# Kernel optimization log

Hardware: AMD Instinct MI355X
Metric: run time of the kernel (lower is better)

## Reference

```python
import jax, jax.numpy as jnp
import numpy as np

N = 50000
E = 800000
C = 128          # in = hidden = out channels
R = 16           # num_relations
NB = 4           # num_bases
EPS = 1e-5


def setup_inputs() -> dict:
    key = jax.random.key(0)
    ks = jax.random.split(key, 20)
    node_features = jax.random.normal(ks[0], (N, C), dtype=jnp.float32)
    src = jax.random.randint(ks[1], (E,), 0, N, dtype=jnp.int32)
    rel = jax.random.randint(ks[2], (E,), 0, R, dtype=jnp.int32)
    dst = jax.random.randint(ks[3], (E,), 0, N, dtype=jnp.int32)
    edge_triples = jnp.stack([src, rel, dst], axis=1)  # [E,3]
    s = 0.05
    inp = {
        "node_features": node_features,
        "edge_triples": edge_triples,
        "num_nodes": N,
        "input_w": jax.random.normal(ks[4], (C, C), jnp.float32) * s,
        "input_b": jnp.zeros((C,), jnp.float32),
    }
    for i in range(2):
        k = jax.random.split(ks[5 + i], 4)
        inp[f"basis{i}"] = jax.random.normal(k[0], (NB, C, C), jnp.float32) * s
        inp[f"att{i}"] = jax.random.normal(k[1], (R, NB), jnp.float32) * s
        inp[f"root_w{i}"] = jax.random.normal(k[2], (C, C), jnp.float32) * s
        inp[f"root_b{i}"] = jnp.zeros((C,), jnp.float32)
        inp[f"ln_g{i}"] = jnp.ones((C,), jnp.float32)
        inp[f"ln_b{i}"] = jnp.zeros((C,), jnp.float32)
    return inp


def _layer_norm(x, g, b):
    mu = jnp.mean(x, axis=-1, keepdims=True)
    var = jnp.mean(jnp.square(x - mu), axis=-1, keepdims=True)
    return (x - mu) * jax.lax.rsqrt(var + EPS) * g + b


def _rel_conv(x, edge_triples, num_nodes, basis, att, root_w, root_b):
    # x: [N,C]; basis: [NB,C,O]; att: [R,NB]
    src = edge_triples[:, 0]
    rel = edge_triples[:, 1]
    dst = edge_triples[:, 2]
    # weights = einsum('rb,bio->rio'); messages_e = x[src] @ weights[rel]
    # = sum_b att[rel,b] * (x @ basis[b])[src]  (same math, no [E,C,O] tensor)
    xb = jnp.einsum('ni,bio->bno', x, basis)      # [NB,N,O]
    coef = att[rel]                                # [E,NB]
    out_dim = basis.shape[-1]
    msg = jnp.zeros((src.shape[0], out_dim), x.dtype)
    for b in range(basis.shape[0]):                # small fixed loop over bases
        msg = msg + coef[:, b, None] * xb[b][src]
    deg = jax.ops.segment_sum(jnp.ones_like(dst, dtype=x.dtype), dst,
                              num_segments=num_nodes)
    deg_inv = jnp.where(deg > 0, 1.0 / deg, 0.0)
    msg = msg * deg_inv[dst][:, None]
    out = jax.ops.segment_sum(msg, dst, num_segments=num_nodes)
    return out + x @ root_w + root_b


def reference(node_features, edge_triples, num_nodes, input_w, input_b,
              basis0, att0, root_w0, root_b0, ln_g0, ln_b0,
              basis1, att1, root_w1, root_b1, ln_g1, ln_b1):
    x = node_features @ input_w + input_b
    x = _rel_conv(x, edge_triples, num_nodes, basis0, att0, root_w0, root_b0)
    x = _layer_norm(x, ln_g0, ln_b0)
    x = jax.nn.relu(x)  # dropout is identity in eval mode
    x = _rel_conv(x, edge_triples, num_nodes, basis1, att1, root_w1, root_b1)
    x = _layer_norm(x, ln_g1, ln_b1)
    return x
```

## Files before the change

### kernel.cpp

```cpp
#include <hip/hip_runtime.h>
#include <hip/hip_bf16.h>
#include <hip/hip_fp8.h>

#define NN 50000
#define EE 800000
#define NBLK 196

typedef __bf16 bf16x8 __attribute__((ext_vector_type(8)));
typedef float f32x4 __attribute__((ext_vector_type(4)));

__device__ inline float bf2f(unsigned int u) {
    union { unsigned int i; float f; } x; x.i = (u & 0xFFFFu) << 16; return x.f;
}
__device__ inline float bf2fh(unsigned int u) {
    union { unsigned int i; float f; } x; x.i = u & 0xFFFF0000u; return x.f;
}
__device__ inline void bf8_to_f(bf16x8 v, float* f) {
    const unsigned int* u = (const unsigned int*)&v;
    f[0] = bf2f(u[0]); f[1] = bf2fh(u[0]);
    f[2] = bf2f(u[1]); f[3] = bf2fh(u[1]);
    f[4] = bf2f(u[2]); f[5] = bf2fh(u[2]);
    f[6] = bf2f(u[3]); f[7] = bf2fh(u[3]);
}

__device__ inline void fp8x8_to_f(uint2 w, float* f) {
#if __has_builtin(__builtin_amdgcn_cvt_f32_fp8)
    f[0] = __builtin_amdgcn_cvt_f32_fp8(w.x, 0);
    f[1] = __builtin_amdgcn_cvt_f32_fp8(w.x, 1);
    f[2] = __builtin_amdgcn_cvt_f32_fp8(w.x, 2);
    f[3] = __builtin_amdgcn_cvt_f32_fp8(w.x, 3);
    f[4] = __builtin_amdgcn_cvt_f32_fp8(w.y, 0);
    f[5] = __builtin_amdgcn_cvt_f32_fp8(w.y, 1);
    f[6] = __builtin_amdgcn_cvt_f32_fp8(w.y, 2);
    f[7] = __builtin_amdgcn_cvt_f32_fp8(w.y, 3);
#else
    const unsigned char* b = (const unsigned char*)&w;
    #pragma unroll
    for (int j = 0; j < 8; ++j) { __hip_fp8_e4m3 v; v.__x = b[j]; f[j] = float(v); }
#endif
}
__device__ inline uint2 f8_pack(const float* f) {
#if __has_builtin(__builtin_amdgcn_cvt_pk_fp8_f32)
    unsigned int lo = __builtin_amdgcn_cvt_pk_fp8_f32(f[0], f[1], 0u, false);
    lo = __builtin_amdgcn_cvt_pk_fp8_f32(f[2], f[3], lo, true);
    unsigned int hi = __builtin_amdgcn_cvt_pk_fp8_f32(f[4], f[5], 0u, false);
    hi = __builtin_amdgcn_cvt_pk_fp8_f32(f[6], f[7], hi, true);
    return make_uint2(lo, hi);
#else
    unsigned char b[8];
    #pragma unroll
    for (int j = 0; j < 8; ++j) { __hip_fp8_e4m3 v(f[j]); b[j] = v.__x; }
    return *(uint2*)b;
#endif
}

__global__ void k_cvt8(const __bf16* __restrict__ in, unsigned char* __restrict__ out, int n8) {
    int i = blockIdx.x * 256 + threadIdx.x;
    if (i >= n8) return;
    bf16x8 v = ((const bf16x8*)in)[i];
    float f[8];
    bf8_to_f(v, f);
    ((uint2*)out)[i] = f8_pack(f);
}

__global__ void k_init(int* __restrict__ deg, int* __restrict__ curs,
                       const float* __restrict__ iw,
                       const float* __restrict__ basis0, const float* __restrict__ rootw0,
                       const float* __restrict__ basis1, const float* __restrict__ rootw1,
                       __bf16* __restrict__ WtInF, __bf16* __restrict__ WtF0, __bf16* __restrict__ WtF1) {
    int idx = blockIdx.x * 256 + threadIdx.x;
    if (idx < NN) { deg[idx] = 0; curs[idx] = 0; }
    int t = idx;
    if (t < 2048) {
        int lane = t & 63, grp = t >> 6;
        int kk = grp & 3, nblk = grp >> 2;
        int col = nblk * 16 + (lane & 15);
        int k0 = kk * 32 + (lane >> 4) * 8;
        bf16x8 v;
        #pragma unroll
        for (int j = 0; j < 8; ++j) v[j] = (__bf16)iw[(size_t)(k0 + j) * 128 + col];
        *(bf16x8*)(WtInF + (size_t)t * 8) = v;
        return;
    }
    t -= 2048;
    const float* basis = basis0; const float* rootw = rootw0; __bf16* W = WtF0;
    if (t >= 10240) { t -= 10240; basis = basis1; rootw = rootw1; W = WtF1; }
    if (t >= 10240) return;
    int lane = t & 63, grp = t >> 6;
    int kk = grp % 20, nblk = grp / 20;
    int col = nblk * 16 + (lane & 15);
    int k0 = kk * 32 + (lane >> 4) * 8;
    bf16x8 v;
    #pragma unroll
    for (int j = 0; j < 8; ++j) {
        int k = k0 + j;
        float f = (k < 512) ? basis[(size_t)(k >> 7) * 16384 + (size_t)(k & 127) * 128 + col]
                            : rootw[(size_t)(k - 512) * 128 + col];
        v[j] = (__bf16)f;
    }
    *(bf16x8*)(W + (size_t)t * 8) = v;
}

__global__ void k_deg4(const int4* __restrict__ et4, int* __restrict__ deg) {
    int t = blockIdx.x * 256 + threadIdx.x;
    if (t >= EE / 4) return;
    int4 a = et4[(size_t)t * 3];
    int4 b = et4[(size_t)t * 3 + 1];
    int4 c = et4[(size_t)t * 3 + 2];
    atomicAdd(&deg[a.z], 1);
    atomicAdd(&deg[b.y], 1);
    atomicAdd(&deg[c.x], 1);
    atomicAdd(&deg[c.w], 1);
}

__global__ void k_scan1(const int* __restrict__ deg, int* __restrict__ incl, int* __restrict__ bsum) {
    __shared__ int s[1024];
    int i = blockIdx.x * 1024 + threadIdx.x;
    int v = (i < NN) ? deg[i] : 0;
    s[threadIdx.x] = v;
    __syncthreads();
    for (int off = 1; off < 1024; off <<= 1) {
        int t = (threadIdx.x >= off) ? s[threadIdx.x - off] : 0;
        __syncthreads();
        s[threadIdx.x] += t;
        __syncthreads();
    }
    if (i < NN) incl[i] = s[threadIdx.x];
    if (threadIdx.x == 1023) bsum[blockIdx.x] = s[1023];
}

__global__ void k_scan3b(const int* __restrict__ incl, const int* __restrict__ deg,
                         const int* __restrict__ bsum, int* __restrict__ row_start) {
    __shared__ int sboff;
    if (threadIdx.x == 0) {
        int a = 0;
        for (int k = 0; k < (int)blockIdx.x; ++k) a += bsum[k];
        sboff = a;
    }
    __syncthreads();
    int i = blockIdx.x * 1024 + threadIdx.x;
    if (i < NN) row_start[i] = incl[i] - deg[i] + sboff;
}

__global__ void k_fill4(const int4* __restrict__ et4, const int* __restrict__ row_start,
                        int* __restrict__ cursor, int* __restrict__ perm) {
    int t = blockIdx.x * 256 + threadIdx.x;
    if (t >= EE / 4) return;
    int4 a = et4[(size_t)t * 3];
    int4 b = et4[(size_t)t * 3 + 1];
    int4 c = et4[(size_t)t * 3 + 2];
    int src[4] = {a.x, a.w, b.z, c.y};
    int rel[4] = {a.y, b.x, b.w, c.z};
    int dst[4] = {a.z, b.y, c.x, c.w};
    #pragma unroll
    for (int j = 0; j < 4; ++j) {
        int pos = row_start[dst[j]] + atomicAdd(&cursor[dst[j]], 1);
        perm[pos] = src[j] | (rel[j] << 16);
    }
}

__global__ void k_gemm_in(const float* __restrict__ A, const __bf16* __restrict__ WtInF,
                          const float* __restrict__ bias, __bf16* __restrict__ out, int M) {
    const int tid = threadIdx.x, wave = tid >> 6, lane = tid & 63;
    const int wr = wave >> 1, wc = wave & 1;
    const int l15 = lane & 15, lhi = lane >> 4;
    f32x4 acc[2][4] = {};
    #define LDAI(dst, KK) do { \
        _Pragma("unroll") \
        for (int m = 0; m < 2; ++m) { \
            int rw = blockIdx.x * 64 + wr * 32 + m * 16 + l15; \
            rw = rw < M ? rw : M - 1; \
            const float* ap = A + (size_t)rw * 128 + (KK) * 32 + lhi * 8; \
            float4 v0 = *(const float4*)ap, v1 = *(const float4*)(ap + 4); \
            bf16x8 f; \
            f[0]=(__bf16)v0.x; f[1]=(__bf16)v0.y; f[2]=(__bf16)v0.z; f[3]=(__bf16)v0.w; \
            f[4]=(__bf16)v1.x; f[5]=(__bf16)v1.y; f[6]=(__bf16)v1.z; f[7]=(__bf16)v1.w; \
            dst[m] = f; \
        } } while (0)
    #define LDBI(dst, KK) do { \
        _Pragma("unroll") \
        for (int n = 0; n < 4; ++n) \
            dst[n] = *(const bf16x8*)(WtInF + (((size_t)(wc * 4 + n) * 4 + (KK)) * 64 + lane) * 8); \
        } while (0)
    #define MMI(AA, BB) do { \
        _Pragma("unroll") for (int m = 0; m < 2; ++m) \
        _Pragma("unroll") for (int n = 0; n < 4; ++n) \
            acc[m][n] = __builtin_amdgcn_mfma_f32_16x16x32_bf16(AA[m], BB[n], acc[m][n], 0, 0, 0); \
        } while (0)
    bf16x8 aP[2], bP[4], aQ[2], bQ[4];
    LDAI(aP, 0); LDBI(bP, 0);
    #pragma unroll
    for (int tstep = 0; tstep < 2; ++tstep) {
        LDAI(aQ, 2 * tstep + 1); LDBI(bQ, 2 * tstep + 1);
        MMI(aP, bP);
        if (tstep < 1) { LDAI(aP, 2 * tstep + 2); LDBI(bP, 2 * tstep + 2); }
        MMI(aQ, bQ);
    }
    #pragma unroll
    for (int m = 0; m < 2; ++m)
        #pragma unroll
        for (int j = 0; j < 4; ++j) {
            int row = blockIdx.x * 64 + wr * 32 + m * 16 + lhi * 4 + j;
            if (row >= M) continue;
            #pragma unroll
            for (int n = 0; n < 4; ++n) {
                int col = wc * 64 + n * 16 + l15;
                out[(size_t)row * 128 + col] = (__bf16)(acc[m][n][j] + bias[col]);
            }
        }
}

__global__ void k_agg7(const unsigned char* __restrict__ x8, const int* __restrict__ perm,
                       const int* __restrict__ rowst, const int* __restrict__ deg,
                       const float* __restrict__ att, __bf16* __restrict__ aggF,
                       int nodeOff, int nodeCnt) {
    __shared__ float4 satt[16];
    if (threadIdx.x < 16) satt[threadIdx.x] = ((const float4*)att)[threadIdx.x];
    __syncthreads();
    int local = blockIdx.x * 4 + (threadIdx.x >> 6);
    if (local >= nodeCnt) return;
    int lane = threadIdx.x & 63;
    int e4 = lane >> 4, c8 = lane & 15;
    int node = nodeOff + local;
    int start = rowst[node], cnt = deg[node];
    float acc[4][8] = {};
    int nIt = (cnt + 3) >> 2;
    for (int it = 0; it < nIt; it += 2) {
        int eA = it * 4 + e4, eB = eA + 4;
        bool vA = eA < cnt, vB = eB < cnt;
        int pA = vA ? perm[start + eA] : 0;
        int pB = vB ? perm[start + eB] : 0;
        uint2 uA = *(const uint2*)(x8 + (size_t)(pA & 0xFFFF) * 128 + c8 * 8);
        uint2 uB = *(const uint2*)(x8 + (size_t)(pB & 0xFFFF) * 128 + c8 * 8);
        float4 cA = vA ? satt[pA >> 16] : make_float4(0.f, 0.f, 0.f, 0.f);
        float4 cB = vB ? satt[pB >> 16] : make_float4(0.f, 0.f, 0.f, 0.f);
        float fA[8], fB[8];
        fp8x8_to_f(uA, fA);
        fp8x8_to_f(uB, fB);
        #pragma unroll
        for (int j = 0; j < 8; ++j) {
            acc[0][j] += cA.x * fA[j]; acc[1][j] += cA.y * fA[j];
            acc[2][j] += cA.z * fA[j]; acc[3][j] += cA.w * fA[j];
        }
        #pragma unroll
        for (int j = 0; j < 8; ++j) {
            acc[0][j] += cB.x * fB[j]; acc[1][j] += cB.y * fB[j];
            acc[2][j] += cB.z * fB[j]; acc[3][j] += cB.w * fB[j];
        }
    }
    float dinv = (cnt > 0) ? 1.f / (float)cnt : 0.f;
    #pragma unroll
    for (int b = 0; b < 4; ++b)
        #pragma unroll
        for (int j = 0; j < 8; ++j) {
            float v = acc[b][j];
            v += __shfl_xor(v, 16);
            v += __shfl_xor(v, 32);
            acc[b][j] = v * dinv;
        }
    bf16x8 o;
    #pragma unroll
    for (int j = 0; j < 8; ++j) {
        float v = (e4 == 0) ? acc[0][j] : (e4 == 1) ? acc[1][j] : (e4 == 2) ? acc[2][j] : acc[3][j];
        o[j] = (__bf16)v;
    }
    size_t idx8 = (((size_t)(local >> 4) * 16 + e4 * 4 + (c8 >> 2)) * 64 + (c8 & 3) * 16 + (local & 15)) * 8;
    *(bf16x8*)(aggF + idx8) = o;
}

template<int OUTF>
__global__ void k_gemm_layer(const __bf16* __restrict__ aggF, const __bf16* __restrict__ x,
                             const __bf16* __restrict__ WtF, const float* __restrict__ rb,
                             const float* __restrict__ g, const float* __restrict__ bb,
                             __bf16* __restrict__ outB, float* __restrict__ outF,
                             int rowOff, int nodeCnt) {
    __shared__ float red[2][2][64];
    __shared__ float murs[2][64];
    const int tid = threadIdx.x, wave = tid >> 6, lane = tid & 63;
    const int wr = wave >> 1, wc = wave & 1;
    const int l15 = lane & 15, lhi = lane >> 4;
    const int rowgrpBase = blockIdx.x * 4 + wr * 2;
    f32x4 acc[2][4] = {};
    #define LDA(dst, KK) do { \
        _Pragma("unroll") \
        for (int m = 0; m < 2; ++m) { \
            if ((KK) < 16) { \
                dst[m] = *(const bf16x8*)(aggF + (((size_t)(rowgrpBase + m) * 16 + (KK)) * 64 + lane) * 8); \
            } else { \
                int rw = blockIdx.x * 64 + wr * 32 + m * 16 + l15; \
                rw = rw < nodeCnt ? rw : nodeCnt - 1; \
                dst[m] = *(const bf16x8*)(x + (size_t)(rowOff + rw) * 128 + ((KK) - 16) * 32 + lhi * 8); \
            } \
        } } while (0)
    #define LDB(dst, KK) do { \
        _Pragma("unroll") \
        for (int n = 0; n < 4; ++n) \
            dst[n] = *(const bf16x8*)(WtF + (((size_t)(wc * 4 + n) * 20 + (KK)) * 64 + lane) * 8); \
        } while (0)
    #define MM(AA, BB) do { \
        _Pragma("unroll") for (int m = 0; m < 2; ++m) \
        _Pragma("unroll") for (int n = 0; n < 4; ++n) \
            acc[m][n] = __builtin_amdgcn_mfma_f32_16x16x32_bf16(AA[m], BB[n], acc[m][n], 0, 0, 0); \
        } while (0)
    bf16x8 aP[2], bP[4], aQ[2], bQ[4];
    LDA(aP, 0); LDB(bP, 0);
    #pragma unroll
    for (int t = 0; t < 10; ++t) {
        LDA(aQ, 2 * t + 1); LDB(bQ, 2 * t + 1);
        MM(aP, bP);
        if (t < 9) { LDA(aP, 2 * t + 2); LDB(bP, 2 * t + 2); }
        MM(aQ, bQ);
    }
    float colb[4];
    #pragma unroll
    for (int n = 0; n < 4; ++n) colb[n] = rb[wc * 64 + n * 16 + l15];
    #pragma unroll
    for (int m = 0; m < 2; ++m)
        #pragma unroll
        for (int j = 0; j < 4; ++j) {
            float s = 0.f, q = 0.f;
            #pragma unroll
            for (int n = 0; n < 4; ++n) {
                float v = acc[m][n][j] + colb[n];
                acc[m][n][j] = v;
                s += v; q += v * v;
            }
            #pragma unroll
            for (int o = 1; o < 16; o <<= 1) { s += __shfl_xor(s, o); q += __shfl_xor(q, o); }
            if (l15 == 0) {
                int r = wr * 32 + m * 16 + lhi * 4 + j;
                red[0][wc][r] = s; red[1][wc][r] = q;
            }
        }
    __syncthreads();
    if (tid < 64) {
        float s = red[0][0][tid] + red[0][1][tid];
        float q = red[1][0][tid] + red[1][1][tid];
        float mu = s * (1.f / 128.f);
        float var = q * (1.f / 128.f) - mu * mu;
        murs[0][tid] = mu;
        murs[1][tid] = rsqrtf(var + 1e-5f);
    }
    __syncthreads();
    float gg[4], gb[4];
    #pragma unroll
    for (int n = 0; n < 4; ++n) {
        int col = wc * 64 + n * 16 + l15;
        gg[n] = g[col]; gb[n] = bb[col];
    }
    #pragma unroll
    for (int m = 0; m < 2; ++m)
        #pragma unroll
        for (int j = 0; j < 4; ++j) {
            int rblk = wr * 32 + m * 16 + lhi * 4 + j;
            int lr = blockIdx.x * 64 + rblk;
            if (lr >= nodeCnt) continue;
            float mu = murs[0][rblk], rs = murs[1][rblk];
            size_t rowbase = (size_t)(rowOff + lr) * 128;
            #pragma unroll
            for (int n = 0; n < 4; ++n) {
                int col = wc * 64 + n * 16 + l15;
                float v = (acc[m][n][j] - mu) * rs * gg[n] + gb[n];
                if (OUTF == 0) { v = fmaxf(v, 0.f); outB[rowbase + col] = (__bf16)v; }
                else           { outF[rowbase + col] = v; }
            }
        }
}

extern "C" void kernel_launch(void* const* d_in, const int* in_sizes, int n_in,
                              void* d_out, int out_size, void* d_ws, size_t ws_size,
                              hipStream_t stream) {
    const float* nf      = (const float*)d_in[0];
    const int*   et      = (const int*)d_in[1];
    const float* input_w = (const float*)d_in[3];
    const float* input_b = (const float*)d_in[4];
    const float* basis0  = (const float*)d_in[5];
    const float* att0    = (const float*)d_in[6];
    const float* rootw0  = (const float*)d_in[7];
    const float* rootb0  = (const float*)d_in[8];
    const float* lng0    = (const float*)d_in[9];
    const float* lnb0    = (const float*)d_in[10];
    const float* basis1  = (const float*)d_in[11];
    const float* att1    = (const float*)d_in[12];
    const float* rootw1  = (const float*)d_in[13];
    const float* rootb1  = (const float*)d_in[14];
    const float* lng1    = (const float*)d_in[15];
    const float* lnb1    = (const float*)d_in[16];
    (void)in_sizes; (void)n_in; (void)out_size;

    char* ws = (char*)d_ws;
    size_t off = 0;
    auto carve = [&](size_t bytes) { char* p = ws + off; off = (off + bytes + 255) & ~(size_t)255; return p; };
    __bf16* x0    = (__bf16*)carve((size_t)NN * 128 * 2);
    __bf16* x1    = (__bf16*)carve((size_t)NN * 128 * 2);
    unsigned char* x08 = (unsigned char*)carve((size_t)NN * 128);
    unsigned char* x18 = (unsigned char*)carve((size_t)NN * 128);
    __bf16* WtInF = (__bf16*)carve((size_t)128 * 128 * 2);
    __bf16* WtF0  = (__bf16*)carve((size_t)128 * 640 * 2);
    __bf16* WtF1  = (__bf16*)carve((size_t)128 * 640 * 2);
    int*    deg   = (int*)carve((size_t)NN * 4);
    int*    incl  = (int*)carve((size_t)NN * 4);
    int*    rowst = (int*)carve((size_t)NN * 4);
    int*    curs  = (int*)carve((size_t)NN * 4);
    int*    bsum  = (int*)carve(64 * 4);
    int*    perm  = (int*)carve((size_t)EE * 4 + 64);
    size_t remain = (ws_size > off + 4096) ? (ws_size - off - 4096) : 0;
    long long maxNodes = (long long)(remain / 1024);
    int chunkN = (maxNodes >= NN) ? NN : (int)maxNodes;
    if (chunkN < 512) chunkN = 512;
    chunkN = (chunkN + 63) & ~63;
    __bf16* aggF = (__bf16*)carve((size_t)chunkN * 512 * 2);
    int nch = (NN + chunkN - 1) / chunkN;

    k_init<<<NBLK, 256, 0, stream>>>(deg, curs, input_w, basis0, rootw0, basis1, rootw1,
                                     WtInF, WtF0, WtF1);
    k_deg4<<<(EE / 4 + 255) / 256, 256, 0, stream>>>((const int4*)et, deg);
    k_scan1<<<49, 1024, 0, stream>>>(deg, incl, bsum);
    k_scan3b<<<49, 1024, 0, stream>>>(incl, deg, bsum, rowst);
    k_fill4<<<(EE / 4 + 255) / 256, 256, 0, stream>>>((const int4*)et, rowst, curs, perm);

    k_gemm_in<<<(NN + 63) / 64, 256, 0, stream>>>(nf, WtInF, input_b, x0, NN);
    k_cvt8<<<(NN * 16 + 255) / 256, 256, 0, stream>>>(x0, x08, NN * 16);

    for (int c = 0; c < nch; ++c) {
        int o0 = c * chunkN;
        int cnt = (o0 + chunkN <= NN) ? chunkN : (NN - o0);
        k_agg7<<<(cnt + 3) / 4, 256, 0, stream>>>(x08, perm, rowst, deg, att0, aggF, o0, cnt);
        k_gemm_layer<0><<<(cnt + 63) / 64, 256, 0, stream>>>(aggF, x0, WtF0, rootb0, lng0, lnb0,
                                                             x1, nullptr, o0, cnt);
    }
    k_cvt8<<<(NN * 16 + 255) / 256, 256, 0, stream>>>(x1, x18, NN * 16);

    for (int c = 0; c < nch; ++c) {
        int o0 = c * chunkN;
        int cnt = (o0 + chunkN <= NN) ? chunkN : (NN - o0);
        k_agg7<<<(cnt + 3) / 4, 256, 0, stream>>>(x18, perm, rowst, deg, att1, aggF, o0, cnt);
        k_gemm_layer<1><<<(cnt + 63) / 64, 256, 0, stream>>>(aggF, x1, WtF1, rootb1, lng1, lnb1,
                                                             nullptr, (float*)d_out, o0, cnt);
    }
}
```

Baseline: 268.6 us.

## Store aggregated features and basis weights in FP8 and use FP8 MFMA

```diff
diff --git a/kernel.cpp b/kernel.cpp
--- a/kernel.cpp
+++ b/kernel.cpp
@@ -67,7 +67,9 @@
                        const float* __restrict__ iw,
                        const float* __restrict__ basis0, const float* __restrict__ rootw0,
                        const float* __restrict__ basis1, const float* __restrict__ rootw1,
-                       __bf16* __restrict__ WtInF, __bf16* __restrict__ WtF0, __bf16* __restrict__ WtF1) {
+                       __bf16* __restrict__ WtInF,
+                       unsigned char* __restrict__ WtF80, __bf16* __restrict__ WtRt0,
+                       unsigned char* __restrict__ WtF81, __bf16* __restrict__ WtRt1) {
     int idx = blockIdx.x * 256 + threadIdx.x;
     if (idx < NN) { deg[idx] = 0; curs[idx] = 0; }
     int t = idx;
@@ -83,22 +85,33 @@
         return;
     }
     t -= 2048;
-    const float* basis = basis0; const float* rootw = rootw0; __bf16* W = WtF0;
-    if (t >= 10240) { t -= 10240; basis = basis1; rootw = rootw1; W = WtF1; }
+    const float* basis = basis0; const float* rootw = rootw0;
+    unsigned char* W8 = WtF80; __bf16* WR = WtRt0;
+    if (t >= 10240) { t -= 10240; basis = basis1; rootw = rootw1; W8 = WtF81; WR = WtRt1; }
     if (t >= 10240) return;
-    int lane = t & 63, grp = t >> 6;
-    int kk = grp % 20, nblk = grp / 20;
-    int col = nblk * 16 + (lane & 15);
-    int k0 = kk * 32 + (lane >> 4) * 8;
-    bf16x8 v;
-    #pragma unroll
-    for (int j = 0; j < 8; ++j) {
-        int k = k0 + j;
-        float f = (k < 512) ? basis[(size_t)(k >> 7) * 16384 + (size_t)(k & 127) * 128 + col]
-                            : rootw[(size_t)(k - 512) * 128 + col];
-        v[j] = (__bf16)f;
-    }
-    *(bf16x8*)(W + (size_t)t * 8) = v;
+    if (t < 8192) {
+        int lane = t & 63, grp = t >> 6;
+        int kk = grp & 15, nblk = grp >> 4;
+        int col = nblk * 16 + (lane & 15);
+        int k0 = kk * 32 + (lane >> 4) * 8;
+        float f[8];
+        #pragma unroll
+        for (int j = 0; j < 8; ++j) {
+            int k = k0 + j;
+            f[j] = 8.0f * basis[(size_t)(k >> 7) * 16384 + (size_t)(k & 127) * 128 + col];
+        }
+        *(uint2*)(W8 + (size_t)t * 8) = f8_pack(f);
+    } else {
+        int t2 = t - 8192;
+        int lane = t2 & 63, grp = t2 >> 6;
+        int kk = grp & 3, nblk = grp >> 2;
+        int col = nblk * 16 + (lane & 15);
+        int k0 = kk * 32 + (lane >> 4) * 8;
+        bf16x8 v;
+        #pragma unroll
+        for (int j = 0; j < 8; ++j) v[j] = (__bf16)rootw[(size_t)(k0 + j) * 128 + col];
+        *(bf16x8*)(WR + (size_t)t2 * 8) = v;
+    }
 }
 
 __global__ void k_deg4(const int4* __restrict__ et4, int* __restrict__ deg) {
@@ -210,10 +223,11 @@
         }
 }
 
-__global__ void k_agg7(const unsigned char* __restrict__ x8, const int* __restrict__ perm,
-                       const int* __restrict__ rowst, const int* __restrict__ deg,
-                       const float* __restrict__ att, __bf16* __restrict__ aggF,
-                       int nodeOff, int nodeCnt) {
+__global__ void __launch_bounds__(256, 8)
+k_agg9(const unsigned char* __restrict__ x8, const int* __restrict__ perm,
+       const int* __restrict__ rowst, const int* __restrict__ deg,
+       const float* __restrict__ att, unsigned char* __restrict__ aggF8,
+       int nodeOff, int nodeCnt) {
     __shared__ float4 satt[16];
     if (threadIdx.x < 16) satt[threadIdx.x] = ((const float4*)att)[threadIdx.x];
     __syncthreads();
@@ -248,7 +262,7 @@
             acc[2][j] += cB.z * fB[j]; acc[3][j] += cB.w * fB[j];
         }
     }
-    float dinv = (cnt > 0) ? 1.f / (float)cnt : 0.f;
+    float dinv8 = (cnt > 0) ? 8.0f / (float)cnt : 0.f;
     #pragma unroll
     for (int b = 0; b < 4; ++b)
         #pragma unroll
@@ -256,21 +270,20 @@
             float v = acc[b][j];
             v += __shfl_xor(v, 16);
             v += __shfl_xor(v, 32);
-            acc[b][j] = v * dinv;
-        }
-    bf16x8 o;
-    #pragma unroll
-    for (int j = 0; j < 8; ++j) {
-        float v = (e4 == 0) ? acc[0][j] : (e4 == 1) ? acc[1][j] : (e4 == 2) ? acc[2][j] : acc[3][j];
-        o[j] = (__bf16)v;
-    }
-    size_t idx8 = (((size_t)(local >> 4) * 16 + e4 * 4 + (c8 >> 2)) * 64 + (c8 & 3) * 16 + (local & 15)) * 8;
-    *(bf16x8*)(aggF + idx8) = o;
+            acc[b][j] = v * dinv8;
+        }
+    float o[8];
+    #pragma unroll
+    for (int j = 0; j < 8; ++j)
+        o[j] = (e4 == 0) ? acc[0][j] : (e4 == 1) ? acc[1][j] : (e4 == 2) ? acc[2][j] : acc[3][j];
+    size_t byteOff = (((size_t)(local >> 4) * 16 + e4 * 4 + (c8 >> 2)) * 64 + (c8 & 3) * 16 + (local & 15)) * 8;
+    *(uint2*)(aggF8 + byteOff) = f8_pack(o);
 }
 
 template<int OUTF>
-__global__ void k_gemm_layer(const __bf16* __restrict__ aggF, const __bf16* __restrict__ x,
-                             const __bf16* __restrict__ WtF, const float* __restrict__ rb,
+__global__ void k_gemm_layer(const unsigned char* __restrict__ aggF8, const __bf16* __restrict__ x,
+                             const unsigned char* __restrict__ WtF8, const __bf16* __restrict__ WtRt,
+                             const float* __restrict__ rb,
                              const float* __restrict__ g, const float* __restrict__ bb,
                              __bf16* __restrict__ outB, float* __restrict__ outF,
                              int rowOff, int nodeCnt) {
@@ -281,35 +294,56 @@
     const int l15 = lane & 15, lhi = lane >> 4;
     const int rowgrpBase = blockIdx.x * 4 + wr * 2;
     f32x4 acc[2][4] = {};
-    #define LDA(dst, KK) do { \
+    #define LD8A(dst, KK) do { \
         _Pragma("unroll") \
-        for (int m = 0; m < 2; ++m) { \
-            if ((KK) < 16) { \
-                dst[m] = *(const bf16x8*)(aggF + (((size_t)(rowgrpBase + m) * 16 + (KK)) * 64 + lane) * 8); \
-            } else { \
-                int rw = blockIdx.x * 64 + wr * 32 + m * 16 + l15; \
-                rw = rw < nodeCnt ? rw : nodeCnt - 1; \
-                dst[m] = *(const bf16x8*)(x + (size_t)(rowOff + rw) * 128 + ((KK) - 16) * 32 + lhi * 8); \
-            } \
-        } } while (0)
-    #define LDB(dst, KK) do { \
+        for (int m = 0; m < 2; ++m) \
+            dst[m] = *(const long*)(aggF8 + (((size_t)(rowgrpBase + m) * 16 + (KK)) * 64 + lane) * 8); \
+        } while (0)
+    #define LD8B(dst, KK) do { \
         _Pragma("unroll") \
         for (int n = 0; n < 4; ++n) \
-            dst[n] = *(const bf16x8*)(WtF + (((size_t)(wc * 4 + n) * 20 + (KK)) * 64 + lane) * 8); \
+            dst[n] = *(const long*)(WtF8 + (((size_t)(wc * 4 + n) * 16 + (KK)) * 64 + lane) * 8); \
         } while (0)
-    #define MM(AA, BB) do { \
+    #define MM8(AA, BB) do { \
         _Pragma("unroll") for (int m = 0; m < 2; ++m) \
         _Pragma("unroll") for (int n = 0; n < 4; ++n) \
-            acc[m][n] = __builtin_amdgcn_mfma_f32_16x16x32_bf16(AA[m], BB[n], acc[m][n], 0, 0, 0); \
+            acc[m][n] = __builtin_amdgcn_mfma_f32_16x16x32_fp8_fp8(AA[m], BB[n], acc[m][n], 0, 0, 0); \
         } while (0)
-    bf16x8 aP[2], bP[4], aQ[2], bQ[4];
-    LDA(aP, 0); LDB(bP, 0);
-    #pragma unroll
-    for (int t = 0; t < 10; ++t) {
-        LDA(aQ, 2 * t + 1); LDB(bQ, 2 * t + 1);
-        MM(aP, bP);
-        if (t < 9) { LDA(aP, 2 * t + 2); LDB(bP, 2 * t + 2); }
-        MM(aQ, bQ);
+    {
+        long aP[2], bP[4], aQ[2], bQ[4];
+        LD8A(aP, 0); LD8B(bP, 0);
+        #pragma unroll
+        for (int t = 0; t < 8; ++t) {
+            LD8A(aQ, 2 * t + 1); LD8B(bQ, 2 * t + 1);
+            MM8(aP, bP);
+            if (t < 7) { LD8A(aP, 2 * t + 2); LD8B(bP, 2 * t + 2); }
+            MM8(aQ, bQ);
+        }
+    }
+    #pragma unroll
+    for (int m = 0; m < 2; ++m)
+        #pragma unroll
+        for (int n = 0; n < 4; ++n)
+            #pragma unroll
+            for (int j = 0; j < 4; ++j)
+                acc[m][n][j] *= 0.015625f;
+    #pragma unroll
+    for (int kk = 0; kk < 4; ++kk) {
+        bf16x8 a[2], b[4];
+        #pragma unroll
+        for (int m = 0; m < 2; ++m) {
+            int rw = blockIdx.x * 64 + wr * 32 + m * 16 + l15;
+            rw = rw < nodeCnt ? rw : nodeCnt - 1;
+            a[m] = *(const bf16x8*)(x + (size_t)(rowOff + rw) * 128 + kk * 32 + lhi * 8);
+        }
+        #pragma unroll
+        for (int n = 0; n < 4; ++n)
+            b[n] = *(const bf16x8*)(WtRt + (((size_t)(wc * 4 + n) * 4 + kk) * 64 + lane) * 8);
+        #pragma unroll
+        for (int m = 0; m < 2; ++m)
+            #pragma unroll
+            for (int n = 0; n < 4; ++n)
+                acc[m][n] = __builtin_amdgcn_mfma_f32_16x16x32_bf16(a[m], b[n], acc[m][n], 0, 0, 0);
     }
     float colb[4];
     #pragma unroll
@@ -396,8 +430,10 @@
     unsigned char* x08 = (unsigned char*)carve((size_t)NN * 128);
     unsigned char* x18 = (unsigned char*)carve((size_t)NN * 128);
     __bf16* WtInF = (__bf16*)carve((size_t)128 * 128 * 2);
-    __bf16* WtF0  = (__bf16*)carve((size_t)128 * 640 * 2);
-    __bf16* WtF1  = (__bf16*)carve((size_t)128 * 640 * 2);
+    unsigned char* WtF80 = (unsigned char*)carve((size_t)512 * 128);
+    __bf16* WtRt0 = (__bf16*)carve((size_t)128 * 128 * 2);
+    unsigned char* WtF81 = (unsigned char*)carve((size_t)512 * 128);
+    __bf16* WtRt1 = (__bf16*)carve((size_t)128 * 128 * 2);
     int*    deg   = (int*)carve((size_t)NN * 4);
     int*    incl  = (int*)carve((size_t)NN * 4);
     int*    rowst = (int*)carve((size_t)NN * 4);
@@ -405,15 +441,15 @@
     int*    bsum  = (int*)carve(64 * 4);
     int*    perm  = (int*)carve((size_t)EE * 4 + 64);
     size_t remain = (ws_size > off + 4096) ? (ws_size - off - 4096) : 0;
-    long long maxNodes = (long long)(remain / 1024);
+    long long maxNodes = (long long)(remain / 512);
     int chunkN = (maxNodes >= NN) ? NN : (int)maxNodes;
     if (chunkN < 512) chunkN = 512;
     chunkN = (chunkN + 63) & ~63;
-    __bf16* aggF = (__bf16*)carve((size_t)chunkN * 512 * 2);
+    unsigned char* aggF8 = (unsigned char*)carve((size_t)chunkN * 512);
     int nch = (NN + chunkN - 1) / chunkN;
 
     k_init<<<NBLK, 256, 0, stream>>>(deg, curs, input_w, basis0, rootw0, basis1, rootw1,
-                                     WtInF, WtF0, WtF1);
+                                     WtInF, WtF80, WtRt0, WtF81, WtRt1);
     k_deg4<<<(EE / 4 + 255) / 256, 256, 0, stream>>>((const int4*)et, deg);
     k_scan1<<<49, 1024, 0, stream>>>(deg, incl, bsum);
     k_scan3b<<<49, 1024, 0, stream>>>(incl, deg, bsum, rowst);
@@ -425,17 +461,17 @@
     for (int c = 0; c < nch; ++c) {
         int o0 = c * chunkN;
         int cnt = (o0 + chunkN <= NN) ? chunkN : (NN - o0);
-        k_agg7<<<(cnt + 3) / 4, 256, 0, stream>>>(x08, perm, rowst, deg, att0, aggF, o0, cnt);
-        k_gemm_layer<0><<<(cnt + 63) / 64, 256, 0, stream>>>(aggF, x0, WtF0, rootb0, lng0, lnb0,
-                                                             x1, nullptr, o0, cnt);
+        k_agg9<<<(cnt + 3) / 4, 256, 0, stream>>>(x08, perm, rowst, deg, att0, aggF8, o0, cnt);
+        k_gemm_layer<0><<<(cnt + 63) / 64, 256, 0, stream>>>(aggF8, x0, WtF80, WtRt0, rootb0,
+                                                             lng0, lnb0, x1, nullptr, o0, cnt);
     }
     k_cvt8<<<(NN * 16 + 255) / 256, 256, 0, stream>>>(x1, x18, NN * 16);
 
     for (int c = 0; c < nch; ++c) {
         int o0 = c * chunkN;
         int cnt = (o0 + chunkN <= NN) ? chunkN : (NN - o0);
-        k_agg7<<<(cnt + 3) / 4, 256, 0, stream>>>(x18, perm, rowst, deg, att1, aggF, o0, cnt);
-        k_gemm_layer<1><<<(cnt + 63) / 64, 256, 0, stream>>>(aggF, x1, WtF1, rootb1, lng1, lnb1,
-                                                             nullptr, (float*)d_out, o0, cnt);
-    }
-}
+        k_agg9<<<(cnt + 3) / 4, 256, 0, stream>>>(x18, perm, rowst, deg, att1, aggF8, o0, cnt);
+        k_gemm_layer<1><<<(cnt + 63) / 64, 256, 0, stream>>>(aggF8, x1, WtF81, WtRt1, rootb1,
+                                                             lng1, lnb1, nullptr, (float*)d_out, o0, cnt);
+    }
+}
```

New measurement: 294.1 us. 1.09x slower.
